# Kernel optimization log

Hardware: AMD Instinct MI355X
Metric: run time of the kernel (lower is better)

Reference implementation:

```python
import jax, jax.numpy as jnp
import numpy as np

N, M, E, F = 100000, 20000, 1000000, 128
LEAKY_SLOPE = 0.2
BN_EPS = 1e-5


def segment_softmax(logits, seg, num_segments):
    # numerically stable softmax over ragged segments
    mx = jax.ops.segment_max(logits, seg, num_segments=num_segments)
    mx = jnp.where(jnp.isfinite(mx), mx, 0.0)  # empty segments -> -inf -> 0
    e = jnp.exp(logits - mx[seg])
    s = jax.ops.segment_sum(e, seg, num_segments=num_segments)
    return e / (s[seg] + 1e-16)


def setup_inputs() -> dict:
    key = jax.random.key(0)
    ks = jax.random.split(key, 6)
    return {
        "x": jax.random.normal(ks[0], (N, F), jnp.float32),
        "hyperedge_attr": jax.random.normal(ks[1], (M, F), jnp.float32),
        "W": jax.random.normal(ks[2], (F, F), jnp.float32) / np.sqrt(F),
        "att": jax.random.normal(ks[3], (2 * F,), jnp.float32) * 0.1,
        "bias": jnp.zeros((F,), jnp.float32),
        "gamma": jnp.ones((F,), jnp.float32),
        "beta": jnp.zeros((F,), jnp.float32),
        "node_idx": jax.random.randint(ks[4], (E,), 0, N, dtype=jnp.int32),
        "edge_idx": jax.random.randint(ks[5], (E,), 0, M, dtype=jnp.int32),
    }


def reference(x, hyperedge_attr, W, att, bias, gamma, beta, node_idx, edge_idx):
    # --- HypergraphConv(use_attention=True, heads=1, attention_mode='node') ---
    xw = x @ W                     # [N, F] transformed node features
    ea = hyperedge_attr @ W        # [M, F] transformed hyperedge features (shared lin)

    # per-incidence attention logits: (cat[x_i, e_j] * att).sum(-1)
    a_node = xw @ att[:F]          # [N]
    a_edge = ea @ att[F:]          # [M]
    alpha = a_node[node_idx] + a_edge[edge_idx]          # [E]
    alpha = jax.nn.leaky_relu(alpha, LEAKY_SLOPE)
    alpha = segment_softmax(alpha, edge_idx, M)          # softmax per hyperedge

    ones = jnp.ones((E,), xw.dtype)
    D = jax.ops.segment_sum(ones, node_idx, num_segments=N)   # node degree
    Dinv = jnp.where(D > 0, 1.0 / D, 0.0)
    Bdeg = jax.ops.segment_sum(ones, edge_idx, num_segments=M)  # hyperedge size
    Binv = jnp.where(Bdeg > 0, 1.0 / Bdeg, 0.0)

    # node -> hyperedge: gather node feats, weight by B^{-1}*alpha, scatter to edges
    m1 = (Binv[edge_idx] * alpha)[:, None] * xw[node_idx]        # [E, F]
    edge_feat = jax.ops.segment_sum(m1, edge_idx, num_segments=M)  # [M, F]

    # hyperedge -> node: gather edge feats, weight by D^{-1}*alpha, scatter to nodes
    m2 = (Dinv[node_idx] * alpha)[:, None] * edge_feat[edge_idx]  # [E, F]
    out = jax.ops.segment_sum(m2, node_idx, num_segments=N) + bias  # [N, F]

    # --- BatchNorm1d (training-mode batch statistics, biased variance) ---
    mu = out.mean(axis=0)
    var = out.var(axis=0)
    out = gamma * (out - mu) * jax.lax.rsqrt(var + BN_EPS) + beta

    # --- ELU, dropout (eval: identity), residual (in_dim == out_dim) ---
    out = jax.nn.elu(out)
    return out + x
```

## Files before the change

### kernel.cpp

```cpp
#include <hip/hip_runtime.h>
#include <hip/hip_bf16.h>

#define NN 100000
#define MM 20000
#define EE 1000000
#define FF 128

#define EBK 157
#define NBK 782
#define ECAP 7168
#define NCAP 1664
#define CHUNK 2048
#define NREP 64

typedef unsigned short u16;
typedef unsigned int u32;
typedef __attribute__((ext_vector_type(8))) short short8v;
typedef __attribute__((ext_vector_type(4))) float f32x4;

__device__ __forceinline__ u16 f2bf(float f) {
  u32 x = __float_as_uint(f);
  return (u16)((x + 0x7FFFu + ((x >> 16) & 1u)) >> 16);
}
__device__ __forceinline__ float bf2f(u16 u) { return __uint_as_float(((u32)u) << 16); }
__device__ __forceinline__ float leaky(float v) { return v > 0.f ? v : 0.2f * v; }
__device__ __forceinline__ float readlane_f(float v, int l) {
  return __uint_as_float((u32)__builtin_amdgcn_readlane((int)__float_as_uint(v), l));
}

__global__ __launch_bounds__(256) void k_prep(const float* __restrict__ W,
                                              const float* __restrict__ att,
                                              float* __restrict__ watt2, u16* __restrict__ WtSwz,
                                              int* __restrict__ ecur, int* __restrict__ ncur,
                                              float* __restrict__ bn_partial) {
  int gid = blockIdx.x * 256 + threadIdx.x;
  if (gid < EBK) ecur[gid] = 0;
  if (gid < NBK) ncur[gid] = 0;
  if (gid < NREP * 256) bn_partial[gid] = 0.f;
  if (blockIdx.x == 0 && threadIdx.x < 128) {
    int t = threadIdx.x;
    float s2 = 0.f;
    for (int c = 0; c < FF; c += 4) {
      float4 wv = *(const float4*)(W + t * FF + c);
      s2 += wv.x * att[FF + c] + wv.y * att[FF + c + 1] + wv.z * att[FF + c + 2] + wv.w * att[FF + c + 3];
    }
    watt2[t] = s2;
    int c = t;
    for (int k = 0; k < FF; k += 2) {
      u32 p = (u32)f2bf(W[k * FF + c]) | ((u32)f2bf(W[(k + 1) * FF + c]) << 16);
      int byte = c * 256 + ((k * 2) ^ ((c & 7) << 4));
      *(u32*)((char*)WtSwz + byte) = p;
    }
  }
}

__global__ __launch_bounds__(256) void k_gemm(const float* __restrict__ x,
                                              const u16* __restrict__ WtSwz,
                                              const float* __restrict__ att,
                                              u16* __restrict__ xw,
                                              float* __restrict__ a_node) {
  __shared__ u16 Wl[FF * FF];
  __shared__ u16 xl[64 * FF];
  int t = threadIdx.x;
  {
    const uint4* src = (const uint4*)WtSwz;
    uint4* dst = (uint4*)Wl;
    for (int i = t; i < FF * FF * 2 / 16; i += 256) dst[i] = src[i];
  }
  int row0 = blockIdx.x * 64;
  for (int chunk = t; chunk < 64 * 32; chunk += 256) {
    int r = chunk >> 5;
    int j = chunk & 31;
    float4 v = make_float4(0.f, 0.f, 0.f, 0.f);
    if (row0 + r < NN) v = ((const float4*)(x + (size_t)(row0 + r) * FF))[j];
    uint2 p;
    p.x = (u32)f2bf(v.x) | ((u32)f2bf(v.y) << 16);
    p.y = (u32)f2bf(v.z) | ((u32)f2bf(v.w) << 16);
    int byte = r * 256 + ((j * 8) ^ ((r & 7) << 4));
    *(uint2*)((char*)xl + byte) = p;
  }
  __syncthreads();

  int wid = t >> 6, lane = t & 63;
  int r_lo = lane & 15, khalf = lane >> 4;
  f32x4 acc[8];
#pragma unroll
  for (int ct = 0; ct < 8; ++ct) acc[ct] = (f32x4){0.f, 0.f, 0.f, 0.f};

#pragma unroll
  for (int kc = 0; kc < 4; ++kc) {
    int kbyte = kc * 64 + khalf * 16;
    int arow = wid * 16 + r_lo;
    short8v a = *(const short8v*)((const char*)xl + arow * 256 + (kbyte ^ ((arow & 7) << 4)));
#pragma unroll
    for (int ct = 0; ct < 8; ++ct) {
      int brow = ct * 16 + r_lo;
      short8v b = *(const short8v*)((const char*)Wl + brow * 256 + (kbyte ^ ((brow & 7) << 4)));
      acc[ct] = __builtin_amdgcn_mfma_f32_16x16x32_bf16(a, b, acc[ct], 0, 0, 0);
    }
  }

  float att_c[8];
#pragma unroll
  for (int ct = 0; ct < 8; ++ct) att_c[ct] = att[ct * 16 + r_lo];
  float p[4] = {0.f, 0.f, 0.f, 0.f};
#pragma unroll
  for (int ct = 0; ct < 8; ++ct) {
#pragma unroll
    for (int reg = 0; reg < 4; ++reg) {
      int lrow = wid * 16 + khalf * 4 + reg;
      int grow = row0 + lrow;
      if (grow < NN) xw[(size_t)grow * FF + ct * 16 + r_lo] = f2bf(acc[ct][reg]);
      p[reg] += acc[ct][reg] * att_c[ct];
    }
  }
#pragma unroll
  for (int off = 1; off <= 8; off <<= 1) {
#pragma unroll
    for (int reg = 0; reg < 4; ++reg) p[reg] += __shfl_xor(p[reg], off, 64);
  }
  if (r_lo == 0) {
#pragma unroll
    for (int reg = 0; reg < 4; ++reg) {
      int grow = row0 + wid * 16 + khalf * 4 + reg;
      if (grow < NN) a_node[grow] = p[reg];
    }
  }
}

__global__ __launch_bounds__(256) void k_aedge(const float* __restrict__ he,
                                               const float* __restrict__ watt2,
                                               float* __restrict__ a_edge) {
  int m = (blockIdx.x * 256 + threadIdx.x) >> 6;
  int lane = threadIdx.x & 63;
  if (m >= MM) return;
  float2 wv = ((const float2*)watt2)[lane];
  float2 v = ((const float2*)(he + (size_t)m * FF))[lane];
  float p = v.x * wv.x + v.y * wv.y;
#pragma unroll
  for (int off = 32; off; off >>= 1) p += __shfl_xor(p, off, 64);
  if (lane == 0) a_edge[m] = p;
}

__global__ __launch_bounds__(256) void k_binA(const int* __restrict__ node_idx,
                                              const int* __restrict__ edge_idx,
                                              int* __restrict__ ecur, int* __restrict__ ncur,
                                              u32* __restrict__ ebins, u32* __restrict__ nbins) {
  __shared__ int ecnt[EBK], ncnt[NBK], ebase[EBK], nbase[NBK];
  int t = threadIdx.x;
  for (int i = t; i < EBK; i += 256) ecnt[i] = 0;
  for (int i = t; i < NBK; i += 256) ncnt[i] = 0;
  __syncthreads();
  int start = blockIdx.x * CHUNK;
  int end = min(start + CHUNK, EE);
  for (int e = start + t; e < end; e += 256) {
    int m = edge_idx[e], n = node_idx[e];
    atomicAdd(&ecnt[m >> 7], 1);
    atomicAdd(&ncnt[n >> 7], 1);
  }
  __syncthreads();
  for (int i = t; i < EBK; i += 256) {
    int c = ecnt[i];
    ebase[i] = c ? atomicAdd(&ecur[i], c) : 0;
    ecnt[i] = 0;
  }
  for (int i = t; i < NBK; i += 256) {
    int c = ncnt[i];
    nbase[i] = c ? atomicAdd(&ncur[i], c) : 0;
    ncnt[i] = 0;
  }
  __syncthreads();
  for (int e = start + t; e < end; e += 256) {
    int m = edge_idx[e], n = node_idx[e];
    int eb = m >> 7, nb = n >> 7;
    int p = ebase[eb] + atomicAdd(&ecnt[eb], 1);
    if (p < ECAP) ebins[(size_t)eb * ECAP + p] = ((u32)n << 7) | (u32)(m & 127);
    int q = nbase[nb] + atomicAdd(&ncnt[nb], 1);
    if (q < NCAP) nbins[(size_t)nb * NCAP + q] = ((u32)m << 7) | (u32)(n & 127);
  }
}

__global__ __launch_bounds__(256) void k_binB(const u32* __restrict__ ebins,
                                              const int* __restrict__ ecur,
                                              int* __restrict__ edge_ptr,
                                              int* __restrict__ csrE_node,
                                              const u32* __restrict__ nbins,
                                              const int* __restrict__ ncur,
                                              int* __restrict__ node_ptr,
                                              int* __restrict__ csrN_edge) {
  __shared__ int cnt[128], cur[128], sc[128];
  __shared__ int ps[256];
  int t = threadIdx.x;
  bool is_edge = blockIdx.x < EBK;
  int b = is_edge ? blockIdx.x : blockIdx.x - EBK;
  const int* curArr = is_edge ? ecur : ncur;
  const u32* src = is_edge ? (ebins + (size_t)b * ECAP) : (nbins + (size_t)b * NCAP);
  int count = is_edge ? min(ecur[b], ECAP) : min(ncur[b], NCAP);
  int* ptr = is_edge ? edge_ptr : node_ptr;
  int* csr = is_edge ? csrE_node : csrN_edge;
  int glen = is_edge ? MM : NN;
  int nbk = is_edge ? EBK : NBK;

  int acc = 0;
  for (int i = t; i < b; i += 256) acc += curArr[i];
  ps[t] = acc;
  __syncthreads();
  for (int off = 128; off; off >>= 1) {
    if (t < off) ps[t] += ps[t + off];
    __syncthreads();
  }
  int gbase = ps[0];

  if (t < 128) cnt[t] = 0;
  __syncthreads();
  for (int i = t; i < count; i += 256) atomicAdd(&cnt[src[i] & 127], 1);
  __syncthreads();
  if (t < 128) sc[t] = cnt[t];
  __syncthreads();
  for (int off = 1; off < 128; off <<= 1) {
    int u = (t >= off && t < 128) ? sc[t - off] : 0;
    __syncthreads();
    if (t < 128) sc[t] += u;
    __syncthreads();
  }
  if (t < 128) {
    int excl = sc[t] - cnt[t];
    cur[t] = excl;
    int g = b * 128 + t;
    if (g < glen) ptr[g] = gbase + excl;
  }
  if (b == nbk - 1 && t == 0) ptr[glen] = gbase + count;
  __syncthreads();
  for (int i = t; i < count; i += 256) {
    u32 v = src[i];
    int pos = atomicAdd(&cur[v & 127], 1);
    csr[gbase + pos] = (int)(v >> 7);
  }
}

__global__ __launch_bounds__(256) void k_edge_agg(const int* __restrict__ edge_ptr,
                                                  const int* __restrict__ csrE_node,
                                                  const float* __restrict__ a_node,
                                                  const float* __restrict__ a_edge,
                                                  const u16* __restrict__ xw,
                                                  u16* __restrict__ edge_feat,
                                                  float2* __restrict__ edge_sc) {
  int m = (blockIdx.x * 256 + threadIdx.x) >> 6;
  int lane = threadIdx.x & 63;
  if (m >= MM) return;
  int s0 = edge_ptr[m], s1 = edge_ptr[m + 1];
  int len = s1 - s0;
  if (len == 0) return;
  float ae = a_edge[m];

  float ssum_l = 0.f;
  float accx = 0.f, accy = 0.f;
  for (int base = s0; base < s1; base += 64) {
    int i = base + lane;
    bool valid = i < s1;
    int n_l = valid ? csrE_node[i] : 0;
    float w_l = valid ? __expf(leaky(a_node[n_l] + ae)) : 0.f;
    ssum_l += w_l;
    int cnt = min(64, s1 - base);
    for (int b = 0; b < cnt; b += 16) {
      u32 u[16];
      float wv[16];
#pragma unroll
      for (int j = 0; j < 16; ++j) {
        int n = __builtin_amdgcn_readlane(n_l, b + j);
        wv[j] = readlane_f(w_l, b + j);
        u[j] = *(const u32*)(xw + (size_t)n * FF + 2 * lane);
      }
#pragma unroll
      for (int j = 0; j < 16; ++j) {
        accx += wv[j] * bf2f((u16)u[j]);
        accy += wv[j] * bf2f((u16)(u[j] >> 16));
      }
    }
  }
#pragma unroll
  for (int off = 1; off < 64; off <<= 1) ssum_l += __shfl_xor(ssum_l, off, 64);
  float invs = 1.0f / (ssum_l + 1e-16f);
  float r = invs / (float)len;
  u32 packed = (u32)f2bf(accx * r) | ((u32)f2bf(accy * r) << 16);
  *(u32*)(edge_feat + (size_t)m * FF + 2 * lane) = packed;
  if (lane == 0) edge_sc[m] = make_float2(ae, invs);
}

__global__ __launch_bounds__(256) void k_node_agg(const int* __restrict__ node_ptr,
                                                  const int* __restrict__ csrN_edge,
                                                  const float* __restrict__ a_node,
                                                  const u16* __restrict__ edge_feat,
                                                  const float2* __restrict__ edge_sc,
                                                  const float* __restrict__ bias,
                                                  float* __restrict__ out_f32,
                                                  u16* __restrict__ raw_bf,
                                                  float* __restrict__ bn_partial) {
  __shared__ float4 sd[4][64];
  int wid = threadIdx.x >> 6, lane = threadIdx.x & 63;
  float2 bv = ((const float2*)bias)[lane];
  float s1x = 0.f, s1y = 0.f, s2x = 0.f, s2y = 0.f;
#pragma unroll
  for (int k = 0; k < 4; ++k) {
    int n = blockIdx.x * 16 + wid * 4 + k;
    int s0 = node_ptr[n], s1 = node_ptr[n + 1];
    float an = a_node[n];
    float accx = 0.f, accy = 0.f;
    for (int base = s0; base < s1; base += 64) {
      int i = base + lane;
      bool valid = i < s1;
      int m_l = valid ? csrN_edge[i] : 0;
      float w_l = 0.f;
      if (valid) {
        float2 sc = edge_sc[m_l];
        w_l = __expf(leaky(an + sc.x)) * sc.y;
      }
      int cnt = min(64, s1 - base);
      for (int b = 0; b < cnt; b += 16) {
        u32 u[16];
        float wv[16];
#pragma unroll
        for (int j = 0; j < 16; ++j) {
          int mm = __builtin_amdgcn_readlane(m_l, b + j);
          wv[j] = readlane_f(w_l, b + j);
          u[j] = *(const u32*)(edge_feat + (size_t)mm * FF + 2 * lane);
        }
#pragma unroll
        for (int j = 0; j < 16; ++j) {
          accx += wv[j] * bf2f((u16)u[j]);
          accy += wv[j] * bf2f((u16)(u[j] >> 16));
        }
      }
    }
    int deg = s1 - s0;
    float dinv = deg > 0 ? 1.0f / (float)deg : 0.f;
    float ox = accx * dinv + bv.x;
    float oy = accy * dinv + bv.y;
    if (raw_bf) {
      *(u32*)(raw_bf + (size_t)n * FF + 2 * lane) = (u32)f2bf(ox) | ((u32)f2bf(oy) << 16);
    } else {
      ((float2*)(out_f32 + (size_t)n * FF))[lane] = make_float2(ox, oy);
    }
    s1x += ox; s1y += oy;
    s2x += ox * ox; s2y += oy * oy;
  }
  sd[wid][lane] = make_float4(s1x, s1y, s2x, s2y);
  __syncthreads();
  if (wid == 0) {
    float4 a0 = sd[0][lane], a1 = sd[1][lane], a2 = sd[2][lane], a3 = sd[3][lane];
    float4 s;
    s.x = a0.x + a1.x + a2.x + a3.x;
    s.y = a0.y + a1.y + a2.y + a3.y;
    s.z = a0.z + a1.z + a2.z + a3.z;
    s.w = a0.w + a1.w + a2.w + a3.w;
    float* bp = bn_partial + (blockIdx.x & (NREP - 1)) * 256;
    atomicAdd(bp + 2 * lane, s.x);
    atomicAdd(bp + 2 * lane + 1, s.y);
    atomicAdd(bp + 128 + 2 * lane, s.z);
    atomicAdd(bp + 128 + 2 * lane + 1, s.w);
  }
}

__global__ void k_bn_final(const float* __restrict__ bn_partial, const float* __restrict__ gamma,
                           const float* __restrict__ beta, float* __restrict__ ss) {
  int c = threadIdx.x;
  float s1 = 0.f, s2 = 0.f;
  for (int r = 0; r < NREP; ++r) {
    s1 += bn_partial[r * 256 + c];
    s2 += bn_partial[r * 256 + 128 + c];
  }
  float mu = s1 * (1.0f / NN);
  float var = s2 * (1.0f / NN) - mu * mu;
  var = fmaxf(var, 0.f);
  float sc = gamma[c] * rsqrtf(var + 1e-5f);
  ss[c] = sc;
  ss[FF + c] = beta[c] - mu * sc;
}

__global__ __launch_bounds__(256) void k_finalize(float* __restrict__ out,
                                                  const u16* __restrict__ raw_bf,
                                                  const float* __restrict__ x,
                                                  const float* __restrict__ ss) {
  int idx = blockIdx.x * 256 + threadIdx.x;
  float4 v;
  if (raw_bf) {
    ushort4 rv = *(const ushort4*)(raw_bf + (size_t)idx * 4);
    v = make_float4(bf2f(rv.x), bf2f(rv.y), bf2f(rv.z), bf2f(rv.w));
  } else {
    v = ((const float4*)out)[idx];
  }
  float4 xr = ((const float4*)x)[idx];
  int cb = (idx * 4) & 127;
  float4 sc = *(const float4*)(ss + cb);
  float4 sh = *(const float4*)(ss + FF + cb);
  v.x = fmaf(v.x, sc.x, sh.x);
  v.y = fmaf(v.y, sc.y, sh.y);
  v.z = fmaf(v.z, sc.z, sh.z);
  v.w = fmaf(v.w, sc.w, sh.w);
  v.x = v.x > 0.f ? v.x : expm1f(v.x);
  v.y = v.y > 0.f ? v.y : expm1f(v.y);
  v.z = v.z > 0.f ? v.z : expm1f(v.z);
  v.w = v.w > 0.f ? v.w : expm1f(v.w);
  v.x += xr.x; v.y += xr.y; v.z += xr.z; v.w += xr.w;
  ((float4*)out)[idx] = v;
}

extern "C" void kernel_launch(void* const* d_in, const int* in_sizes, int n_in,
                              void* d_out, int out_size, void* d_ws, size_t ws_size,
                              hipStream_t stream) {
  const float* x     = (const float*)d_in[0];
  const float* he    = (const float*)d_in[1];
  const float* W     = (const float*)d_in[2];
  const float* att   = (const float*)d_in[3];
  const float* bias  = (const float*)d_in[4];
  const float* gamma = (const float*)d_in[5];
  const float* beta  = (const float*)d_in[6];
  const int* node_idx = (const int*)d_in[7];
  const int* edge_idx = (const int*)d_in[8];
  float* out = (float*)d_out;

  char* w = (char*)d_ws;
  auto alloc = [&](size_t bytes) -> char* {
    char* p = w;
    w += (bytes + 255) & ~(size_t)255;
    return p;
  };
  u16*   xw        = (u16*)  alloc((size_t)NN * FF * 2);
  float* a_node    = (float*)alloc((size_t)NN * 4);
  float* a_edge    = (float*)alloc((size_t)MM * 4);
  u16*   WtSwz     = (u16*)  alloc((size_t)FF * FF * 2);
  float* watt2     = (float*)alloc(FF * 4);
  u16*   edge_feat = (u16*)  alloc((size_t)MM * FF * 2);
  float2* edge_sc  = (float2*)alloc((size_t)MM * 8);
  int* edge_ptr    = (int*)  alloc((size_t)(MM + 1) * 4);
  int* node_ptr    = (int*)  alloc((size_t)(NN + 1) * 4);
  int* csrE_node   = (int*)  alloc((size_t)EE * 4);
  int* csrN_edge   = (int*)  alloc((size_t)EE * 4);
  int* ecur        = (int*)  alloc((size_t)EBK * 4);
  int* ncur        = (int*)  alloc((size_t)NBK * 4);
  u32* ebins       = (u32*)  alloc((size_t)EBK * ECAP * 4);
  u32* nbins       = (u32*)  alloc((size_t)NBK * NCAP * 4);
  float* bn_partial= (float*)alloc((size_t)NREP * 256 * 4);
  float* ss        = (float*)alloc(2 * FF * 4);
  u16*   raw_cand  = (u16*)  alloc((size_t)NN * FF * 2);
  size_t need = (size_t)(w - (char*)d_ws);
  u16* raw_bf = (need <= ws_size) ? raw_cand : (u16*)nullptr;

  k_prep<<<64, 256, 0, stream>>>(W, att, watt2, WtSwz, ecur, ncur, bn_partial);
  k_gemm<<<(NN + 63) / 64, 256, 0, stream>>>(x, WtSwz, att, xw, a_node);
  k_aedge<<<(MM * 64 + 255) / 256, 256, 0, stream>>>(he, watt2, a_edge);

  k_binA<<<(EE + CHUNK - 1) / CHUNK, 256, 0, stream>>>(node_idx, edge_idx, ecur, ncur, ebins, nbins);
  k_binB<<<EBK + NBK, 256, 0, stream>>>(ebins, ecur, edge_ptr, csrE_node,
                                        nbins, ncur, node_ptr, csrN_edge);

  k_edge_agg<<<(MM + 3) / 4, 256, 0, stream>>>(edge_ptr, csrE_node, a_node, a_edge, xw, edge_feat, edge_sc);
  k_node_agg<<<NN / 16, 256, 0, stream>>>(node_ptr, csrN_edge, a_node, edge_feat, edge_sc, bias, out, raw_bf, bn_partial);
  k_bn_final<<<1, 128, 0, stream>>>(bn_partial, gamma, beta, ss);
  k_finalize<<<(NN * FF / 4 + 255) / 256, 256, 0, stream>>>(out, raw_bf, x, ss);
}
```

Measured before the change: 206.0 us.

## Precompute unnormalized attention weights during CSR build; shrink GEMM row tile

The CSR scatter kernel now computes exp(leaky(a_node+a_edge)) for each incidence and stores it alongside the CSR indices for both orientations. The edge and node aggregation kernels then read these weights instead of gathering a_node and a_edge and recomputing the exponential. The node pass now needs only a per-edge inverse sum. The GEMM row tile also drops from 64 to 32 rows, with the four waves split across rows and column halves and the attention dot reduced through shared memory. This adds two E-sized float arrays of extra traffic and removes the bounds checks, which relies on N being divisible by 32.

Result: no change. 202.5 us (-1.7%).

```diff
diff --git a/kernel.cpp b/kernel.cpp
--- a/kernel.cpp
+++ b/kernel.cpp
@@ -12,6 +12,7 @@
 #define NCAP 1664
 #define CHUNK 2048
 #define NREP 64
+#define BM 32
 
 typedef unsigned short u16;
 typedef unsigned int u32;
@@ -60,19 +61,20 @@
                                               u16* __restrict__ xw,
                                               float* __restrict__ a_node) {
   __shared__ u16 Wl[FF * FF];
-  __shared__ u16 xl[64 * FF];
+  __shared__ u16 xl[BM * FF];
+  __shared__ float pn[BM];
   int t = threadIdx.x;
   {
     const uint4* src = (const uint4*)WtSwz;
     uint4* dst = (uint4*)Wl;
     for (int i = t; i < FF * FF * 2 / 16; i += 256) dst[i] = src[i];
   }
-  int row0 = blockIdx.x * 64;
-  for (int chunk = t; chunk < 64 * 32; chunk += 256) {
+  if (t < BM) pn[t] = 0.f;
+  int row0 = blockIdx.x * BM;
+  for (int chunk = t; chunk < BM * 32; chunk += 256) {
     int r = chunk >> 5;
     int j = chunk & 31;
-    float4 v = make_float4(0.f, 0.f, 0.f, 0.f);
-    if (row0 + r < NN) v = ((const float4*)(x + (size_t)(row0 + r) * FF))[j];
+    float4 v = ((const float4*)(x + (size_t)(row0 + r) * FF))[j];
     uint2 p;
     p.x = (u32)f2bf(v.x) | ((u32)f2bf(v.y) << 16);
     p.y = (u32)f2bf(v.z) | ((u32)f2bf(v.w) << 16);
@@ -82,35 +84,35 @@
   __syncthreads();
 
   int wid = t >> 6, lane = t & 63;
+  int rt = wid & 1, ch = wid >> 1;
   int r_lo = lane & 15, khalf = lane >> 4;
-  f32x4 acc[8];
-#pragma unroll
-  for (int ct = 0; ct < 8; ++ct) acc[ct] = (f32x4){0.f, 0.f, 0.f, 0.f};
+  f32x4 acc[4];
+#pragma unroll
+  for (int ct = 0; ct < 4; ++ct) acc[ct] = (f32x4){0.f, 0.f, 0.f, 0.f};
 
 #pragma unroll
   for (int kc = 0; kc < 4; ++kc) {
     int kbyte = kc * 64 + khalf * 16;
-    int arow = wid * 16 + r_lo;
+    int arow = rt * 16 + r_lo;
     short8v a = *(const short8v*)((const char*)xl + arow * 256 + (kbyte ^ ((arow & 7) << 4)));
 #pragma unroll
-    for (int ct = 0; ct < 8; ++ct) {
-      int brow = ct * 16 + r_lo;
+    for (int ct = 0; ct < 4; ++ct) {
+      int brow = ch * 64 + ct * 16 + r_lo;
       short8v b = *(const short8v*)((const char*)Wl + brow * 256 + (kbyte ^ ((brow & 7) << 4)));
       acc[ct] = __builtin_amdgcn_mfma_f32_16x16x32_bf16(a, b, acc[ct], 0, 0, 0);
     }
   }
 
-  float att_c[8];
-#pragma unroll
-  for (int ct = 0; ct < 8; ++ct) att_c[ct] = att[ct * 16 + r_lo];
+  float att_c[4];
+#pragma unroll
+  for (int ct = 0; ct < 4; ++ct) att_c[ct] = att[ch * 64 + ct * 16 + r_lo];
   float p[4] = {0.f, 0.f, 0.f, 0.f};
 #pragma unroll
-  for (int ct = 0; ct < 8; ++ct) {
+  for (int ct = 0; ct < 4; ++ct) {
 #pragma unroll
     for (int reg = 0; reg < 4; ++reg) {
-      int lrow = wid * 16 + khalf * 4 + reg;
-      int grow = row0 + lrow;
-      if (grow < NN) xw[(size_t)grow * FF + ct * 16 + r_lo] = f2bf(acc[ct][reg]);
+      int lrow = rt * 16 + khalf * 4 + reg;
+      xw[(size_t)(row0 + lrow) * FF + ch * 64 + ct * 16 + r_lo] = f2bf(acc[ct][reg]);
       p[reg] += acc[ct][reg] * att_c[ct];
     }
   }
@@ -121,11 +123,11 @@
   }
   if (r_lo == 0) {
 #pragma unroll
-    for (int reg = 0; reg < 4; ++reg) {
-      int grow = row0 + wid * 16 + khalf * 4 + reg;
-      if (grow < NN) a_node[grow] = p[reg];
-    }
-  }
+    for (int reg = 0; reg < 4; ++reg)
+      atomicAdd(&pn[rt * 16 + khalf * 4 + reg], p[reg]);
+  }
+  __syncthreads();
+  if (t < BM) a_node[row0 + t] = pn[t];
 }
 
 __global__ __launch_bounds__(256) void k_aedge(const float* __restrict__ he,
@@ -184,12 +186,17 @@
                                               const int* __restrict__ ecur,
                                               int* __restrict__ edge_ptr,
                                               int* __restrict__ csrE_node,
+                                              float* __restrict__ uwE,
                                               const u32* __restrict__ nbins,
                                               const int* __restrict__ ncur,
                                               int* __restrict__ node_ptr,
-                                              int* __restrict__ csrN_edge) {
+                                              int* __restrict__ csrN_edge,
+                                              float* __restrict__ uwN,
+                                              const float* __restrict__ a_node,
+                                              const float* __restrict__ a_edge) {
   __shared__ int cnt[128], cur[128], sc[128];
   __shared__ int ps[256];
+  __shared__ float loc[128];
   int t = threadIdx.x;
   bool is_edge = blockIdx.x < EBK;
   int b = is_edge ? blockIdx.x : blockIdx.x - EBK;
@@ -198,8 +205,15 @@
   int count = is_edge ? min(ecur[b], ECAP) : min(ncur[b], NCAP);
   int* ptr = is_edge ? edge_ptr : node_ptr;
   int* csr = is_edge ? csrE_node : csrN_edge;
+  float* uwArr = is_edge ? uwE : uwN;
+  const float* gatherA = is_edge ? a_node : a_edge;
   int glen = is_edge ? MM : NN;
   int nbk = is_edge ? EBK : NBK;
+
+  if (t < 128) {
+    int g = b * 128 + t;
+    loc[t] = (g < glen) ? (is_edge ? a_edge[g] : a_node[g]) : 0.f;
+  }
 
   int acc = 0;
   for (int i = t; i < b; i += 256) acc += curArr[i];
@@ -233,25 +247,26 @@
   __syncthreads();
   for (int i = t; i < count; i += 256) {
     u32 v = src[i];
-    int pos = atomicAdd(&cur[v & 127], 1);
-    csr[gbase + pos] = (int)(v >> 7);
+    int lo = v & 127;
+    int other = (int)(v >> 7);
+    int pos = atomicAdd(&cur[lo], 1);
+    csr[gbase + pos] = other;
+    uwArr[gbase + pos] = __expf(leaky(gatherA[other] + loc[lo]));
   }
 }
 
 __global__ __launch_bounds__(256) void k_edge_agg(const int* __restrict__ edge_ptr,
                                                   const int* __restrict__ csrE_node,
-                                                  const float* __restrict__ a_node,
-                                                  const float* __restrict__ a_edge,
+                                                  const float* __restrict__ uwE,
                                                   const u16* __restrict__ xw,
                                                   u16* __restrict__ edge_feat,
-                                                  float2* __restrict__ edge_sc) {
+                                                  float* __restrict__ invsE) {
   int m = (blockIdx.x * 256 + threadIdx.x) >> 6;
   int lane = threadIdx.x & 63;
   if (m >= MM) return;
   int s0 = edge_ptr[m], s1 = edge_ptr[m + 1];
   int len = s1 - s0;
   if (len == 0) return;
-  float ae = a_edge[m];
 
   float ssum_l = 0.f;
   float accx = 0.f, accy = 0.f;
@@ -259,7 +274,7 @@
     int i = base + lane;
     bool valid = i < s1;
     int n_l = valid ? csrE_node[i] : 0;
-    float w_l = valid ? __expf(leaky(a_node[n_l] + ae)) : 0.f;
+    float w_l = valid ? uwE[i] : 0.f;
     ssum_l += w_l;
     int cnt = min(64, s1 - base);
     for (int b = 0; b < cnt; b += 16) {
@@ -284,14 +299,14 @@
   float r = invs / (float)len;
   u32 packed = (u32)f2bf(accx * r) | ((u32)f2bf(accy * r) << 16);
   *(u32*)(edge_feat + (size_t)m * FF + 2 * lane) = packed;
-  if (lane == 0) edge_sc[m] = make_float2(ae, invs);
+  if (lane == 0) invsE[m] = invs;
 }
 
 __global__ __launch_bounds__(256) void k_node_agg(const int* __restrict__ node_ptr,
                                                   const int* __restrict__ csrN_edge,
-                                                  const float* __restrict__ a_node,
+                                                  const float* __restrict__ uwN,
+                                                  const float* __restrict__ invsE,
                                                   const u16* __restrict__ edge_feat,
-                                                  const float2* __restrict__ edge_sc,
                                                   const float* __restrict__ bias,
                                                   float* __restrict__ out_f32,
                                                   u16* __restrict__ raw_bf,
@@ -304,17 +319,12 @@
   for (int k = 0; k < 4; ++k) {
     int n = blockIdx.x * 16 + wid * 4 + k;
     int s0 = node_ptr[n], s1 = node_ptr[n + 1];
-    float an = a_node[n];
     float accx = 0.f, accy = 0.f;
     for (int base = s0; base < s1; base += 64) {
       int i = base + lane;
       bool valid = i < s1;
       int m_l = valid ? csrN_edge[i] : 0;
-      float w_l = 0.f;
-      if (valid) {
-        float2 sc = edge_sc[m_l];
-        w_l = __expf(leaky(an + sc.x)) * sc.y;
-      }
+      float w_l = valid ? uwN[i] * invsE[m_l] : 0.f;
       int cnt = min(64, s1 - base);
       for (int b = 0; b < cnt; b += 16) {
         u32 u[16];
@@ -431,11 +441,13 @@
   u16*   WtSwz     = (u16*)  alloc((size_t)FF * FF * 2);
   float* watt2     = (float*)alloc(FF * 4);
   u16*   edge_feat = (u16*)  alloc((size_t)MM * FF * 2);
-  float2* edge_sc  = (float2*)alloc((size_t)MM * 8);
+  float* invsE     = (float*)alloc((size_t)MM * 4);
   int* edge_ptr    = (int*)  alloc((size_t)(MM + 1) * 4);
   int* node_ptr    = (int*)  alloc((size_t)(NN + 1) * 4);
   int* csrE_node   = (int*)  alloc((size_t)EE * 4);
   int* csrN_edge   = (int*)  alloc((size_t)EE * 4);
+  float* uwE       = (float*)alloc((size_t)EE * 4);
+  float* uwN       = (float*)alloc((size_t)EE * 4);
   int* ecur        = (int*)  alloc((size_t)EBK * 4);
   int* ncur        = (int*)  alloc((size_t)NBK * 4);
   u32* ebins       = (u32*)  alloc((size_t)EBK * ECAP * 4);
@@ -447,15 +459,16 @@
   u16* raw_bf = (need <= ws_size) ? raw_cand : (u16*)nullptr;
 
   k_prep<<<64, 256, 0, stream>>>(W, att, watt2, WtSwz, ecur, ncur, bn_partial);
-  k_gemm<<<(NN + 63) / 64, 256, 0, stream>>>(x, WtSwz, att, xw, a_node);
+  k_gemm<<<NN / BM, 256, 0, stream>>>(x, WtSwz, att, xw, a_node);
   k_aedge<<<(MM * 64 + 255) / 256, 256, 0, stream>>>(he, watt2, a_edge);
 
   k_binA<<<(EE + CHUNK - 1) / CHUNK, 256, 0, stream>>>(node_idx, edge_idx, ecur, ncur, ebins, nbins);
-  k_binB<<<EBK + NBK, 256, 0, stream>>>(ebins, ecur, edge_ptr, csrE_node,
-                                        nbins, ncur, node_ptr, csrN_edge);
-
-  k_edge_agg<<<(MM + 3) / 4, 256, 0, stream>>>(edge_ptr, csrE_node, a_node, a_edge, xw, edge_feat, edge_sc);
-  k_node_agg<<<NN / 16, 256, 0, stream>>>(node_ptr, csrN_edge, a_node, edge_feat, edge_sc, bias, out, raw_bf, bn_partial);
+  k_binB<<<EBK + NBK, 256, 0, stream>>>(ebins, ecur, edge_ptr, csrE_node, uwE,
+                                        nbins, ncur, node_ptr, csrN_edge, uwN,
+                                        a_node, a_edge);
+
+  k_edge_agg<<<(MM + 3) / 4, 256, 0, stream>>>(edge_ptr, csrE_node, uwE, xw, edge_feat, invsE);
+  k_node_agg<<<NN / 16, 256, 0, stream>>>(node_ptr, csrN_edge, uwN, invsE, edge_feat, bias, out, raw_bf, bn_partial);
   k_bn_final<<<1, 128, 0, stream>>>(bn_partial, gamma, beta, ss);
   k_finalize<<<(NN * FF / 4 + 255) / 256, 256, 0, stream>>>(out, raw_bf, x, ss);
 }
```
